# Kernel tuning notes

Measured on AMD Instinct MI355X. Metric: run time of the kernel, lower is better.

## Reference

```python
import jax, jax.numpy as jnp
import numpy as np

B, N = 256, 8192
H = 30
NUM_CLASSES = 5


def setup_inputs() -> dict:
    key = jax.random.key(0)
    ks = jax.random.split(key, 16)
    def dense(k, fi, fo):
        # flax default: lecun_normal kernel, zero bias
        return jax.random.normal(k, (fi, fo), jnp.float32) / jnp.sqrt(fi)
    return {
        'x':   jax.random.normal(ks[0], (B, N), jnp.float32),
        'W1':  dense(ks[1], 1, H),   'b1': jnp.zeros((H,), jnp.float32),
        'W2':  dense(ks[2], H, H),   'b2': jnp.zeros((H,), jnp.float32),
        'Wa1': dense(ks[3], H, 32),  'ba1': jnp.zeros((32,), jnp.float32),
        'Wa2': dense(ks[4], 32, 1),  'ba2': jnp.zeros((1,), jnp.float32),
        'Wf1': dense(ks[5], 6 * H, 40), 'bf1': jnp.zeros((40,), jnp.float32),
        'Wf2': dense(ks[6], 40, 40),    'bf2': jnp.zeros((40,), jnp.float32),
        'Wf3': dense(ks[7], 40, NUM_CLASSES), 'bf3': jnp.zeros((NUM_CLASSES,), jnp.float32),
    }


def reference(x, W1, b1, W2, b2, Wa1, ba1, Wa2, ba2, Wf1, bf1, Wf2, bf2, Wf3, bf3):
    # (B, N) -> (B, N, 1) -> Dense(30) -> relu -> Dense(30)
    h = jax.nn.relu(x[..., None] * W1[0] + b1)          # (B, N, 30)
    h = jnp.einsum('bnh,hk->bnk', h, W2) + b2           # (B, N, 30)

    # statistical pools over the point axis (axis=1)
    mean_pool = jnp.mean(h, axis=1)
    max_pool = jnp.max(h, axis=1)
    min_pool = jnp.min(h, axis=1)
    std_pool = jnp.std(h, axis=1)
    sum_pool = jnp.sum(h, axis=1)

    # attention pooling over points
    a = jax.nn.relu(jnp.einsum('bnh,hk->bnk', h, Wa1) + ba1)  # (B, N, 32)
    logits = jnp.einsum('bnk,ko->bno', a, Wa2) + ba2          # (B, N, 1)
    attn = jax.nn.softmax(logits, axis=1)                     # (B, N, 1)
    attention_pool = jnp.sum(h * attn, axis=1)                # (B, 30)

    feat = jnp.concatenate(
        [mean_pool, max_pool, min_pool, std_pool, sum_pool, attention_pool],
        axis=-1)                                              # (B, 180)

    z = jax.nn.relu(feat @ Wf1 + bf1)
    z = jax.nn.relu(z @ Wf2 + bf2)
    return z @ Wf3 + bf3                                      # (B, num_classes)
```

## Files before the change

kernel.cpp:

```cpp
#include <hip/hip_runtime.h>
#include <math.h>

#define NN 8192
#define HH 30
#define TPB 512
#define NIV 31
#define TSTR 68

__launch_bounds__(TPB, 2)
__global__ void pointnet_pwl5_kernel(
    const float* __restrict__ x,
    const float* __restrict__ W1,  const float* __restrict__ b1,
    const float* __restrict__ W2,  const float* __restrict__ b2,
    const float* __restrict__ Wa1, const float* __restrict__ ba1,
    const float* __restrict__ Wa2, const float* __restrict__ ba2,
    const float* __restrict__ Wf1, const float* __restrict__ bf1,
    const float* __restrict__ Wf2, const float* __restrict__ bf2,
    const float* __restrict__ Wf3, const float* __restrict__ bf3,
    float* __restrict__ out)
{
    __shared__ float W2s[HH][32];
    __shared__ float Wa1s[HH][32];
    __shared__ float w1s[HH], b1s[HH], b2s[32], ba1s[32];
    __shared__ __align__(16) float ts_s[32];
    __shared__ __align__(16) float Wa2s[32];
    __shared__ float tts[HH];
    __shared__ int   rnk[HH];
    __shared__ int   DcS, rmap1S;
    __shared__ float d0S;
    __shared__ float P[HH][32];
    __shared__ float vb2[32];
    __shared__ __align__(16) float ab2[2][64];
    __shared__ __align__(16) float uv2[2][64];
    __shared__ float zz_raw[128], zz_s[128];
    __shared__ float2 gcs[129];
    __shared__ __align__(16) float abt[NIV][TSTR];
    __shared__ __align__(16) float uvt[NIV][TSTR];
    __shared__ float red[8][154];
    __shared__ float fin[16];
    __shared__ float feat[192];
    __shared__ float redh[12][40];
    __shared__ float z1s[40], z2s[40];
    __shared__ float wf2s[40 * 40];
    __shared__ float wf3s[40 * 5];

    const int tid = threadIdx.x;
    const int b   = blockIdx.x;

    float2 xl[8];
    {
        const float2* xb2 = reinterpret_cast<const float2*>(x + (size_t)b * NN);
        #pragma unroll
        for (int it = 0; it < 8; ++it) xl[it] = xb2[it * TPB + tid];
    }
    float wf1r[15];
    if (tid < 480) {
        int o = tid % 40, p = tid / 40;
        const float* wrow = Wf1 + (p * 15) * 40 + o;
        #pragma unroll
        for (int ii = 0; ii < 15; ++ii) wf1r[ii] = wrow[ii * 40];
    }
    float bf1r = 0.f, bf2r = 0.f, bf3r = 0.f;
    if (tid < 40) { bf1r = bf1[tid]; bf2r = bf2[tid]; }
    if (tid < 5)  { bf3r = bf3[tid]; }

    for (int i = tid; i < HH * 32; i += TPB) {
        int j = i >> 5, k = i & 31;
        W2s[j][k] = (k < HH) ? W2[j * HH + k] : 0.f;
    }
    for (int i = tid; i < HH * 32; i += TPB) ((float*)Wa1s)[i] = Wa1[i];
    if (tid < HH) {
        float w = W1[tid], bb = b1[tid];
        w1s[tid] = w; b1s[tid] = bb;
        tts[tid] = (w != 0.f) ? (-bb / w) : INFINITY;
    }
    if (tid < 32) {
        b2s[tid]  = (tid < HH) ? b2[tid] : 0.f;
        ba1s[tid] = ba1[tid];
        Wa2s[tid] = Wa2[tid];
        ts_s[tid] = INFINITY;
    }
    for (int i = tid; i < 40 * 40; i += TPB) wf2s[i] = Wf2[i];
    for (int i = tid; i < 40 * 5;  i += TPB) wf3s[i] = Wf3[i];
    const float ba2v = ba2[0];
    __syncthreads();

    if (tid < HH) {
        float t = tts[tid];
        int r = 0;
        for (int i = 0; i < HH; ++i) {
            float ti = tts[i];
            r += (ti < t) || (ti == t && i < tid);
        }
        ts_s[r] = t;
        rnk[tid] = r;
    } else if (tid >= 32) {
        for (int e = tid - 32; e < HH * 32 + 32; e += (TPB - 32)) {
            if (e < HH * 32) {
                int j = e >> 5, m = e & 31;
                float s = 0.f;
                for (int k = 0; k < HH; ++k) s = fmaf(W2s[j][k], Wa1s[k][m], s);
                P[j][m] = s;
            } else {
                int m = e - HH * 32;
                float s = 0.f;
                for (int k = 0; k < HH; ++k) s = fmaf(Wa1s[k][m], b2s[k], s);
                vb2[m] = s;
            }
        }
    }
    __syncthreads();

    if (tid < 64) {
        bool fin_t = (tid < HH) && (ts_s[tid] < INFINITY);
        bool neq = fin_t && (tid == 0 || ts_s[tid] != ts_s[tid - 1]);
        unsigned long long md = __ballot(neq);
        float t0v = ts_s[0];
        bool eq0 = fin_t && (ts_s[tid] == t0v);
        unsigned long long me = __ballot(eq0);
        if (tid == 0) {
            DcS = __popcll(md);
            d0S = t0v;
            int c2 = __popcll(me);
            rmap1S = (c2 > 30) ? 30 : c2;
        }
    }
    __syncthreads();
    const int Dc = DcS;

    if (Dc == 1) {
        const float d0 = d0S;
        const int rmap1 = rmap1S;

        if (tid < 64) {
            int r = tid >> 5, k = tid & 31;
            int rr = r ? rmap1 : 0;
            float a = 0.f, bb = 0.f;
            if (k < HH) {
                for (int j = 0; j < HH; ++j) {
                    float w = w1s[j];
                    bool act = (w > 0.f) ? (rnk[j] < rr)
                             : ((w < 0.f) ? (rnk[j] >= rr) : (b1s[j] > 0.f));
                    if (act) {
                        float w2 = W2s[j][k];
                        a  = fmaf(w,      w2, a);
                        bb = fmaf(b1s[j], w2, bb);
                    }
                }
                bb += b2s[k];
            }
            ab2[r][k]      = a;
            ab2[r][32 + k] = bb;
        } else if (tid < 128) {
            int i2 = tid - 64;
            int r = i2 >> 5, m = i2 & 31;
            int rr = r ? rmap1 : 0;
            float u = 0.f, v = 0.f;
            for (int j = 0; j < HH; ++j) {
                float w = w1s[j];
                bool act = (w > 0.f) ? (rnk[j] < rr)
                         : ((w < 0.f) ? (rnk[j] >= rr) : (b1s[j] > 0.f));
                if (act) {
                    float pj = P[j][m];
                    u = fmaf(w,      pj, u);
                    v = fmaf(b1s[j], pj, v);
                }
            }
            v += vb2[m] + ba1s[m];
            uv2[r][m]      = u;
            uv2[r][32 + m] = v;
            float zr = -v / u;
            bool ok = (u != 0.f) && (r == 0 ? (zr < d0) : (zr > d0));
            zz_raw[1 + i2] = ok ? zr : INFINITY;
        } else if (tid < 191) {
            zz_raw[tid - 63] = INFINITY;
        } else if (tid == 191) {
            zz_raw[0] = d0;
        }
        __syncthreads();

        if (tid < 128) {
            float v = zz_raw[tid];
            int rk = 0;
            for (int i = 0; i < 128; ++i) {
                float vi = zz_raw[i];
                rk += (vi < v) || (vi == v && i < tid);
            }
            zz_s[rk] = v;
        }
        __syncthreads();

        if (tid < 129) {
            float lo = (tid == 0)   ? -INFINITY : zz_s[tid - 1];
            float hi = (tid == 128) ?  INFINITY : zz_s[tid];
            float xm;
            if (lo == -INFINITY)      xm = (hi < INFINITY) ? hi - 1.f : 0.f;
            else if (hi == INFINITY)  xm = lo + 1.f;
            else                      xm = 0.5f * (lo + hi);
            int r = (xm >= d0) ? 1 : 0;
            float g = 0.f, c = ba2v;
            for (int m = 0; m < 32; ++m) {
                float u = uv2[r][m], v = uv2[r][32 + m];
                if (fmaf(u, xm, v) > 0.f) {
                    float w = Wa2s[m];
                    g = fmaf(w, u, g);
                    c = fmaf(w, v, c);
                }
            }
            gcs[tid] = make_float2(g, c);
        }
        __syncthreads();

        float c0=0,c1=0, Sx0=0,Sx1=0, Q0=0,Q1=0;
        float mn0=INFINITY,mn1=INFINITY, mx0=-INFINITY,mx1=-INFINITY;
        float Sp0=0,Sp1=0, Px0=0,Px1=0;
        float mrun = -INFINITY;

        #pragma unroll
        for (int it = 0; it < 8; ++it) {
            float xv2[2] = { xl[it].x, xl[it].y };
            #pragma unroll
            for (int pp = 0; pp < 2; ++pp) {
                float xv = xv2[pp];
                bool q1 = (xv >= d0);
                int idx = 0;
                #pragma unroll
                for (int bit = 64; bit >= 1; bit >>= 1) {
                    int t = idx + bit;
                    idx = (zz_s[t - 1] <= xv) ? t : idx;
                }
                float2 gc = gcs[idx];
                float l = fmaf(xv, gc.x, gc.y);
                float dlt = l - mrun, p;
                if (dlt > 8.f) {
                    float sc = __expf(-dlt);
                    Sp0 *= sc; Sp1 *= sc; Px0 *= sc; Px1 *= sc;
                    mrun = l; p = 1.f;
                } else p = __expf(dlt);
                float xx = xv * xv, px = p * xv;
                float i1 = q1 ? 1.f : 0.f, i0 = 1.f - i1;
                c0 += i0;                    c1 += i1;
                Sx0 = fmaf(i0, xv, Sx0);     Sx1 = fmaf(i1, xv, Sx1);
                Q0  = fmaf(i0, xx, Q0);      Q1  = fmaf(i1, xx, Q1);
                Sp0 = fmaf(i0, p,  Sp0);     Sp1 = fmaf(i1, p,  Sp1);
                Px0 = fmaf(i0, px, Px0);     Px1 = fmaf(i1, px, Px1);
                mn0 = fminf(mn0, q1 ?  INFINITY : xv);
                mx0 = fmaxf(mx0, q1 ? -INFINITY : xv);
                mn1 = fminf(mn1, q1 ? xv :  INFINITY);
                mx1 = fmaxf(mx1, q1 ? xv : -INFINITY);
            }
        }

        #pragma unroll 1
        for (int off = 32; off > 0; off >>= 1) {
            c0  += __shfl_xor(c0,  off);  c1  += __shfl_xor(c1,  off);
            Sx0 += __shfl_xor(Sx0, off);  Sx1 += __shfl_xor(Sx1, off);
            Q0  += __shfl_xor(Q0,  off);  Q1  += __shfl_xor(Q1,  off);
            mn0 = fminf(mn0, __shfl_xor(mn0, off));
            mn1 = fminf(mn1, __shfl_xor(mn1, off));
            mx0 = fmaxf(mx0, __shfl_xor(mx0, off));
            mx1 = fmaxf(mx1, __shfl_xor(mx1, off));
            float mo = __shfl_xor(mrun, off);
            float M  = fmaxf(mrun, mo);
            float sa = __expf(mrun - M), sb = __expf(mo - M);
            float t;
            t = __shfl_xor(Sp0, off); Sp0 = Sp0 * sa + t * sb;
            t = __shfl_xor(Sp1, off); Sp1 = Sp1 * sa + t * sb;
            t = __shfl_xor(Px0, off); Px0 = Px0 * sa + t * sb;
            t = __shfl_xor(Px1, off); Px1 = Px1 * sa + t * sb;
            mrun = M;
        }

        const int wave = tid >> 6, lane = tid & 63;
        if (lane == 0) {
            float* rw = red[wave];
            rw[0]=c0; rw[1]=Sx0; rw[2]=Q0; rw[3]=mn0; rw[4]=mx0; rw[5]=Sp0; rw[6]=Px0;
            rw[7]=c1; rw[8]=Sx1; rw[9]=Q1; rw[10]=mn1; rw[11]=mx1; rw[12]=Sp1; rw[13]=Px1;
            rw[14]=mrun;
        }
        __syncthreads();

        if (tid < 2) {
            float M = red[0][14];
            #pragma unroll
            for (int w = 1; w < 8; ++w) M = fmaxf(M, red[w][14]);
            int base = tid * 7;
            float ck=0, Sx=0, Q=0, mnv=INFINITY, mxv=-INFINITY, Sp=0, Px=0;
            #pragma unroll
            for (int w = 0; w < 8; ++w) {
                ck += red[w][base+0]; Sx += red[w][base+1]; Q += red[w][base+2];
                mnv = fminf(mnv, red[w][base+3]); mxv = fmaxf(mxv, red[w][base+4]);
                float e = __expf(red[w][14] - M);
                Sp = fmaf(red[w][base+5], e, Sp);
                Px = fmaf(red[w][base+6], e, Px);
            }
            fin[base+0]=ck; fin[base+1]=Sx; fin[base+2]=Q;
            fin[base+3]=mnv; fin[base+4]=mxv; fin[base+5]=Sp; fin[base+6]=Px;
        }
        __syncthreads();

        if (tid < HH) {
            float sumk=0, ssqk=0, acck=0, L=0;
            float mxk=-INFINITY, mnk=INFINITY;
            #pragma unroll
            for (int r2 = 0; r2 < 2; ++r2) {
                float ck = fin[r2*7+0], Sx = fin[r2*7+1], Q = fin[r2*7+2];
                float xmn = fin[r2*7+3], xmx = fin[r2*7+4];
                float Sp = fin[r2*7+5], Px = fin[r2*7+6];
                float a = ab2[r2][tid], bb = ab2[r2][32 + tid];
                sumk += a * Sx + bb * ck;
                ssqk += a * a * Q + 2.f * a * bb * Sx + bb * bb * ck;
                acck += a * Px + bb * Sp;
                L += Sp;
                if (ck > 0.f) {
                    float h1 = fmaf(a, xmn, bb), h2v = fmaf(a, xmx, bb);
                    mxk = fmaxf(mxk, fmaxf(h1, h2v));
                    mnk = fminf(mnk, fminf(h1, h2v));
                }
            }
            const float invN = 1.f / (float)NN;
            float mean = sumk * invN;
            float var  = fmaxf(ssqk * invN - mean * mean, 0.f);
            feat[tid]        = mean;
            feat[30 + tid]   = mxk;
            feat[60 + tid]   = mnk;
            feat[90 + tid]   = sqrtf(var);
            feat[120 + tid]  = sumk;
            feat[150 + tid]  = acck / L;
        }
    } else {
        for (int idx = tid; idx < NIV * 32; idx += TPB) {
            int r = idx >> 5, k = idx & 31;
            float a = 0.f, bb = 0.f;
            if (k < HH) {
                for (int j = 0; j < HH; ++j) {
                    float w = w1s[j];
                    bool act = (w > 0.f) ? (rnk[j] < r)
                             : ((w < 0.f) ? (rnk[j] >= r) : (b1s[j] > 0.f));
                    if (act) {
                        float w2 = W2s[j][k];
                        a  = fmaf(w,      w2, a);
                        bb = fmaf(b1s[j], w2, bb);
                    }
                }
                bb += b2s[k];
            }
            abt[r][k]      = a;
            abt[r][32 + k] = bb;
        }
        __syncthreads();
        for (int idx = tid; idx < NIV * 32; idx += TPB) {
            int r = idx >> 5, m = idx & 31;
            float u = 0.f, v = 0.f;
            for (int k = 0; k < HH; ++k) {
                float wa = Wa1s[k][m];
                u = fmaf(wa, abt[r][k],      u);
                v = fmaf(wa, abt[r][32 + k], v);
            }
            v += ba1s[m];
            uvt[r][m]      = u;
            uvt[r][32 + m] = v;
        }
        __syncthreads();

        float sum[HH], ssq[HH], mx[HH], mn[HH], acc[HH];
        #pragma unroll
        for (int k = 0; k < HH; ++k) {
            sum[k] = 0.f; ssq[k] = 0.f; acc[k] = 0.f;
            mx[k] = -INFINITY; mn[k] = INFINITY;
        }
        float mrun = -INFINITY, lrun = 0.f;
        const float* xb = x + (size_t)b * NN;
        const float4* ts4 = (const float4*)ts_s;
        const float4* wv4 = (const float4*)Wa2s;

        #pragma unroll 1
        for (int it = 0; it < NN / TPB; ++it) {
            float xv = xb[it * TPB + tid];
            int r = 0;
            #pragma unroll
            for (int i = 0; i < 8; ++i) {
                float4 t = ts4[i];
                r += (xv >= t.x) ? 1 : 0;
                r += (xv >= t.y) ? 1 : 0;
                r += (xv >= t.z) ? 1 : 0;
                r += (xv >= t.w) ? 1 : 0;
            }
            float h2[HH];
            const float4* arow = (const float4*)(&abt[r][0]);
            #pragma unroll
            for (int i = 0; i < 7; ++i) {
                float4 av = arow[i], bv = arow[8 + i];
                h2[4*i+0] = fmaf(xv, av.x, bv.x);
                h2[4*i+1] = fmaf(xv, av.y, bv.y);
                h2[4*i+2] = fmaf(xv, av.z, bv.z);
                h2[4*i+3] = fmaf(xv, av.w, bv.w);
            }
            { float4 av = arow[7], bv = arow[15];
              h2[28] = fmaf(xv, av.x, bv.x);
              h2[29] = fmaf(xv, av.y, bv.y); }
            #pragma unroll
            for (int k = 0; k < HH; ++k) {
                float h = h2[k];
                sum[k] += h;
                ssq[k] = fmaf(h, h, ssq[k]);
                mx[k] = fmaxf(mx[k], h);
                mn[k] = fminf(mn[k], h);
            }
            float l = ba2v;
            const float4* urow = (const float4*)(&uvt[r][0]);
            #pragma unroll
            for (int i = 0; i < 8; ++i) {
                float4 uu = urow[i], vv = urow[8 + i], ww = wv4[i];
                l = fmaf(fmaxf(fmaf(xv, uu.x, vv.x), 0.f), ww.x, l);
                l = fmaf(fmaxf(fmaf(xv, uu.y, vv.y), 0.f), ww.y, l);
                l = fmaf(fmaxf(fmaf(xv, uu.z, vv.z), 0.f), ww.z, l);
                l = fmaf(fmaxf(fmaf(xv, uu.w, vv.w), 0.f), ww.w, l);
            }
            float d = l - mrun, p;
            if (d > 8.f) {
                float s = __expf(-d);
                lrun *= s;
                #pragma unroll
                for (int k = 0; k < HH; ++k) acc[k] *= s;
                mrun = l; p = 1.f;
            } else p = __expf(d);
            lrun += p;
            #pragma unroll
            for (int k = 0; k < HH; ++k) acc[k] = fmaf(p, h2[k], acc[k]);
        }

        #pragma unroll 1
        for (int off = 32; off > 0; off >>= 1) {
            #pragma unroll
            for (int k = 0; k < HH; ++k) {
                sum[k] += __shfl_xor(sum[k], off);
                ssq[k] += __shfl_xor(ssq[k], off);
                mx[k] = fmaxf(mx[k], __shfl_xor(mx[k], off));
                mn[k] = fminf(mn[k], __shfl_xor(mn[k], off));
            }
            float mo = __shfl_xor(mrun, off);
            float lo = __shfl_xor(lrun, off);
            float M  = fmaxf(mrun, mo);
            float sa = __expf(mrun - M), sb = __expf(mo - M);
            lrun = lrun * sa + lo * sb;
            #pragma unroll
            for (int k = 0; k < HH; ++k)
                acc[k] = acc[k] * sa + __shfl_xor(acc[k], off) * sb;
            mrun = M;
        }

        const int wave = tid >> 6, lane = tid & 63;
        if (lane == 0) {
            #pragma unroll
            for (int k = 0; k < HH; ++k) {
                red[wave][k]       = sum[k];
                red[wave][30 + k]  = ssq[k];
                red[wave][60 + k]  = mx[k];
                red[wave][90 + k]  = mn[k];
                red[wave][120 + k] = acc[k];
            }
            red[wave][150] = mrun;
            red[wave][151] = lrun;
        }
        __syncthreads();

        if (tid < HH) {
            float M = -INFINITY;
            #pragma unroll
            for (int w = 0; w < 8; ++w) M = fmaxf(M, red[w][150]);
            float s = 0.f, ss = 0.f, L = 0.f, A = 0.f;
            float mxv = -INFINITY, mnv = INFINITY;
            #pragma unroll
            for (int w = 0; w < 8; ++w) {
                s  += red[w][tid];
                ss += red[w][30 + tid];
                mxv = fmaxf(mxv, red[w][60 + tid]);
                mnv = fminf(mnv, red[w][90 + tid]);
                float e = __expf(red[w][150] - M);
                L = fmaf(red[w][151], e, L);
                A = fmaf(red[w][120 + tid], e, A);
            }
            const float invN = 1.f / (float)NN;
            float mean = s * invN;
            float var  = fmaxf(ss * invN - mean * mean, 0.f);
            feat[tid]       = mean;
            feat[30 + tid]  = mxv;
            feat[60 + tid]  = mnv;
            feat[90 + tid]  = sqrtf(var);
            feat[120 + tid] = s;
            feat[150 + tid] = A / L;
        }
    }
    __syncthreads();

    if (tid < 480) {
        int o = tid % 40, p = tid / 40;
        float z = 0.f;
        #pragma unroll
        for (int ii = 0; ii < 15; ++ii)
            z = fmaf(feat[p * 15 + ii], wf1r[ii], z);
        redh[p][o] = z;
    }
    __syncthreads();
    if (tid < 40) {
        float z = bf1r;
        #pragma unroll
        for (int p = 0; p < 12; ++p) z += redh[p][tid];
        z1s[tid] = fmaxf(z, 0.f);
    }
    __syncthreads();
    if (tid < 40) {
        float z = bf2r;
        #pragma unroll
        for (int i = 0; i < 40; ++i) z = fmaf(z1s[i], wf2s[i * 40 + tid], z);
        z2s[tid] = fmaxf(z, 0.f);
    }
    __syncthreads();
    if (tid < 5) {
        float o = bf3r;
        #pragma unroll
        for (int i = 0; i < 40; ++i) o = fmaf(z2s[i], wf3s[i * 5 + tid], o);
        out[b * 5 + tid] = o;
    }
}

extern "C" void kernel_launch(void* const* d_in, const int* in_sizes, int n_in,
                              void* d_out, int out_size, void* d_ws, size_t ws_size,
                              hipStream_t stream) {
    const float* x   = (const float*)d_in[0];
    const float* W1  = (const float*)d_in[1];
    const float* b1  = (const float*)d_in[2];
    const float* W2  = (const float*)d_in[3];
    const float* b2  = (const float*)d_in[4];
    const float* Wa1 = (const float*)d_in[5];
    const float* ba1 = (const float*)d_in[6];
    const float* Wa2 = (const float*)d_in[7];
    const float* ba2 = (const float*)d_in[8];
    const float* Wf1 = (const float*)d_in[9];
    const float* bf1 = (const float*)d_in[10];
    const float* Wf2 = (const float*)d_in[11];
    const float* bf2 = (const float*)d_in[12];
    const float* Wf3 = (const float*)d_in[13];
    const float* bf3 = (const float*)d_in[14];
    float* out = (float*)d_out;

    pointnet_pwl5_kernel<<<256, TPB, 0, stream>>>(
        x, W1, b1, W2, b2, Wa1, ba1, Wa2, ba2,
        Wf1, bf1, Wf2, bf2, Wf3, bf3, out);
}
```

Baseline: 118.6 us.

## Double block size to 1024 threads and simplify single-breakpoint setup path

Raises threads per block from 512 to 1024, so each thread holds 8 points loaded as two float4s and the cross-wave reductions cover 16 waves. The breakpoint setup is simplified: min/max shuffles detect the single-breakpoint case, the rank sort moves into the general path only, and the activation masks no longer use ranks. Wf1 and the final biases are staged in shared memory rather than registers. The aim is more parallelism per sample and a shorter serial prologue, at the cost of larger LDS use, more register pressure per thread and fewer resident blocks per CU.

```diff
diff --git a/kernel.cpp b/kernel.cpp
--- a/kernel.cpp
+++ b/kernel.cpp
@@ -3,12 +3,12 @@
 
 #define NN 8192
 #define HH 30
-#define TPB 512
+#define TPB 1024
 #define NIV 31
 #define TSTR 68
 
-__launch_bounds__(TPB, 2)
-__global__ void pointnet_pwl5_kernel(
+__launch_bounds__(TPB)
+__global__ void pointnet_pwl7_kernel(
     const float* __restrict__ x,
     const float* __restrict__ W1,  const float* __restrict__ b1,
     const float* __restrict__ W2,  const float* __restrict__ b2,
@@ -21,54 +21,47 @@
 {
     __shared__ float W2s[HH][32];
     __shared__ float Wa1s[HH][32];
-    __shared__ float w1s[HH], b1s[HH], b2s[32], ba1s[32];
-    __shared__ __align__(16) float ts_s[32];
-    __shared__ __align__(16) float Wa2s[32];
-    __shared__ float tts[HH];
-    __shared__ int   rnk[HH];
-    __shared__ int   DcS, rmap1S;
+    __shared__ float P[HH][32];
+    __shared__ float w1s[HH], b1s[HH], tts[HH];
+    __shared__ float b2s[32], ba1s[32], Wa2s[32], vb2[32];
+    __shared__ int   DcS;
     __shared__ float d0S;
-    __shared__ float P[HH][32];
-    __shared__ float vb2[32];
     __shared__ __align__(16) float ab2[2][64];
     __shared__ __align__(16) float uv2[2][64];
     __shared__ float zz_raw[128], zz_s[128];
     __shared__ float2 gcs[129];
+    __shared__ __align__(16) float ts_s[32];
+    __shared__ int   rnk[HH];
     __shared__ __align__(16) float abt[NIV][TSTR];
     __shared__ __align__(16) float uvt[NIV][TSTR];
-    __shared__ float red[8][154];
+    __shared__ float redb[16][155];
     __shared__ float fin[16];
     __shared__ float feat[192];
     __shared__ float redh[12][40];
     __shared__ float z1s[40], z2s[40];
+    __shared__ float wf1s[180 * 40];
     __shared__ float wf2s[40 * 40];
     __shared__ float wf3s[40 * 5];
+    __shared__ float bf1s[40], bf2s[40], bf3s[8];
 
     const int tid = threadIdx.x;
     const int b   = blockIdx.x;
 
-    float2 xl[8];
+    float4 xl0, xl1;
     {
-        const float2* xb2 = reinterpret_cast<const float2*>(x + (size_t)b * NN);
-        #pragma unroll
-        for (int it = 0; it < 8; ++it) xl[it] = xb2[it * TPB + tid];
-    }
-    float wf1r[15];
-    if (tid < 480) {
-        int o = tid % 40, p = tid / 40;
-        const float* wrow = Wf1 + (p * 15) * 40 + o;
-        #pragma unroll
-        for (int ii = 0; ii < 15; ++ii) wf1r[ii] = wrow[ii * 40];
-    }
-    float bf1r = 0.f, bf2r = 0.f, bf3r = 0.f;
-    if (tid < 40) { bf1r = bf1[tid]; bf2r = bf2[tid]; }
-    if (tid < 5)  { bf3r = bf3[tid]; }
+        const float4* xb4 = reinterpret_cast<const float4*>(x + (size_t)b * NN);
+        xl0 = xb4[tid];
+        xl1 = xb4[tid + TPB];
+    }
 
     for (int i = tid; i < HH * 32; i += TPB) {
         int j = i >> 5, k = i & 31;
         W2s[j][k] = (k < HH) ? W2[j * HH + k] : 0.f;
     }
     for (int i = tid; i < HH * 32; i += TPB) ((float*)Wa1s)[i] = Wa1[i];
+    for (int i = tid; i < 180 * 40; i += TPB) wf1s[i] = Wf1[i];
+    for (int i = tid; i < 40 * 40;  i += TPB) wf2s[i] = Wf2[i];
+    if (tid < 40 * 5) wf3s[tid] = Wf3[tid];
     if (tid < HH) {
         float w = W1[tid], bb = b1[tid];
         w1s[tid] = w; b1s[tid] = bb;
@@ -80,67 +73,52 @@
         Wa2s[tid] = Wa2[tid];
         ts_s[tid] = INFINITY;
     }
-    for (int i = tid; i < 40 * 40; i += TPB) wf2s[i] = Wf2[i];
-    for (int i = tid; i < 40 * 5;  i += TPB) wf3s[i] = Wf3[i];
+    if (tid < 40) { bf1s[tid] = bf1[tid]; bf2s[tid] = bf2[tid]; }
+    if (tid < 5)  { bf3s[tid] = bf3[tid]; }
     const float ba2v = ba2[0];
     __syncthreads();
 
-    if (tid < HH) {
-        float t = tts[tid];
-        int r = 0;
-        for (int i = 0; i < HH; ++i) {
-            float ti = tts[i];
-            r += (ti < t) || (ti == t && i < tid);
-        }
-        ts_s[r] = t;
-        rnk[tid] = r;
-    } else if (tid >= 32) {
-        for (int e = tid - 32; e < HH * 32 + 32; e += (TPB - 32)) {
-            if (e < HH * 32) {
-                int j = e >> 5, m = e & 31;
-                float s = 0.f;
-                for (int k = 0; k < HH; ++k) s = fmaf(W2s[j][k], Wa1s[k][m], s);
-                P[j][m] = s;
-            } else {
-                int m = e - HH * 32;
-                float s = 0.f;
-                for (int k = 0; k < HH; ++k) s = fmaf(Wa1s[k][m], b2s[k], s);
-                vb2[m] = s;
-            }
+    if (tid < HH * 32) {
+        int j = tid >> 5, m = tid & 31;
+        float s = 0.f;
+        #pragma unroll
+        for (int k = 0; k < HH; ++k) s = fmaf(W2s[j][k], Wa1s[k][m], s);
+        P[j][m] = s;
+    } else if (tid < HH * 32 + 32) {
+        int m = tid - HH * 32;
+        float s = 0.f;
+        #pragma unroll
+        for (int k = 0; k < HH; ++k) s = fmaf(Wa1s[k][m], b2s[k], s);
+        vb2[m] = s;
+    }
+    if (tid < 64) {
+        float t = (tid < HH) ? tts[tid] : INFINITY;
+        bool fin_t = (t < INFINITY);
+        float tmin = fin_t ? t :  INFINITY;
+        float tmax = fin_t ? t : -INFINITY;
+        #pragma unroll
+        for (int off = 32; off > 0; off >>= 1) {
+            tmin = fminf(tmin, __shfl_xor(tmin, off));
+            tmax = fmaxf(tmax, __shfl_xor(tmax, off));
+        }
+        if (tid == 0) {
+            bool dc1 = (tmin < INFINITY) && (tmin == tmax);
+            DcS = dc1 ? 1 : 0;
+            d0S = tmin;
         }
     }
     __syncthreads();
 
-    if (tid < 64) {
-        bool fin_t = (tid < HH) && (ts_s[tid] < INFINITY);
-        bool neq = fin_t && (tid == 0 || ts_s[tid] != ts_s[tid - 1]);
-        unsigned long long md = __ballot(neq);
-        float t0v = ts_s[0];
-        bool eq0 = fin_t && (ts_s[tid] == t0v);
-        unsigned long long me = __ballot(eq0);
-        if (tid == 0) {
-            DcS = __popcll(md);
-            d0S = t0v;
-            int c2 = __popcll(me);
-            rmap1S = (c2 > 30) ? 30 : c2;
-        }
-    }
-    __syncthreads();
-    const int Dc = DcS;
-
-    if (Dc == 1) {
+    if (DcS == 1) {
         const float d0 = d0S;
-        const int rmap1 = rmap1S;
 
         if (tid < 64) {
             int r = tid >> 5, k = tid & 31;
-            int rr = r ? rmap1 : 0;
             float a = 0.f, bb = 0.f;
             if (k < HH) {
                 for (int j = 0; j < HH; ++j) {
                     float w = w1s[j];
-                    bool act = (w > 0.f) ? (rnk[j] < rr)
-                             : ((w < 0.f) ? (rnk[j] >= rr) : (b1s[j] > 0.f));
+                    bool act = (w == 0.f) ? (b1s[j] > 0.f) : (r ? (w > 0.f) : (w < 0.f));
                     if (act) {
                         float w2 = W2s[j][k];
                         a  = fmaf(w,      w2, a);
@@ -154,12 +132,10 @@
         } else if (tid < 128) {
             int i2 = tid - 64;
             int r = i2 >> 5, m = i2 & 31;
-            int rr = r ? rmap1 : 0;
             float u = 0.f, v = 0.f;
             for (int j = 0; j < HH; ++j) {
                 float w = w1s[j];
-                bool act = (w > 0.f) ? (rnk[j] < rr)
-                         : ((w < 0.f) ? (rnk[j] >= rr) : (b1s[j] > 0.f));
+                bool act = (w == 0.f) ? (b1s[j] > 0.f) : (r ? (w > 0.f) : (w < 0.f));
                 if (act) {
                     float pj = P[j][m];
                     u = fmaf(w,      pj, u);
@@ -216,39 +192,36 @@
         float Sp0=0,Sp1=0, Px0=0,Px1=0;
         float mrun = -INFINITY;
 
-        #pragma unroll
-        for (int it = 0; it < 8; ++it) {
-            float xv2[2] = { xl[it].x, xl[it].y };
-            #pragma unroll
-            for (int pp = 0; pp < 2; ++pp) {
-                float xv = xv2[pp];
-                bool q1 = (xv >= d0);
-                int idx = 0;
-                #pragma unroll
-                for (int bit = 64; bit >= 1; bit >>= 1) {
-                    int t = idx + bit;
-                    idx = (zz_s[t - 1] <= xv) ? t : idx;
-                }
-                float2 gc = gcs[idx];
-                float l = fmaf(xv, gc.x, gc.y);
-                float dlt = l - mrun, p;
-                if (dlt > 8.f) {
-                    float sc = __expf(-dlt);
-                    Sp0 *= sc; Sp1 *= sc; Px0 *= sc; Px1 *= sc;
-                    mrun = l; p = 1.f;
-                } else p = __expf(dlt);
-                float xx = xv * xv, px = p * xv;
-                float i1 = q1 ? 1.f : 0.f, i0 = 1.f - i1;
-                c0 += i0;                    c1 += i1;
-                Sx0 = fmaf(i0, xv, Sx0);     Sx1 = fmaf(i1, xv, Sx1);
-                Q0  = fmaf(i0, xx, Q0);      Q1  = fmaf(i1, xx, Q1);
-                Sp0 = fmaf(i0, p,  Sp0);     Sp1 = fmaf(i1, p,  Sp1);
-                Px0 = fmaf(i0, px, Px0);     Px1 = fmaf(i1, px, Px1);
-                mn0 = fminf(mn0, q1 ?  INFINITY : xv);
-                mx0 = fmaxf(mx0, q1 ? -INFINITY : xv);
-                mn1 = fminf(mn1, q1 ? xv :  INFINITY);
-                mx1 = fmaxf(mx1, q1 ? xv : -INFINITY);
-            }
+        float xs[8] = {xl0.x, xl0.y, xl0.z, xl0.w, xl1.x, xl1.y, xl1.z, xl1.w};
+        #pragma unroll
+        for (int pp = 0; pp < 8; ++pp) {
+            float xv = xs[pp];
+            bool q1 = (xv >= d0);
+            int idx = 0;
+            #pragma unroll
+            for (int bit = 64; bit >= 1; bit >>= 1) {
+                int t = idx + bit;
+                idx = (zz_s[t - 1] <= xv) ? t : idx;
+            }
+            float2 gc = gcs[idx];
+            float l = fmaf(xv, gc.x, gc.y);
+            float dlt = l - mrun, p;
+            if (dlt > 8.f) {
+                float sc = __expf(-dlt);
+                Sp0 *= sc; Sp1 *= sc; Px0 *= sc; Px1 *= sc;
+                mrun = l; p = 1.f;
+            } else p = __expf(dlt);
+            float xx = xv * xv, px = p * xv;
+            float i1 = q1 ? 1.f : 0.f, i0 = 1.f - i1;
+            c0 += i0;                    c1 += i1;
+            Sx0 = fmaf(i0, xv, Sx0);     Sx1 = fmaf(i1, xv, Sx1);
+            Q0  = fmaf(i0, xx, Q0);      Q1  = fmaf(i1, xx, Q1);
+            Sp0 = fmaf(i0, p,  Sp0);     Sp1 = fmaf(i1, p,  Sp1);
+            Px0 = fmaf(i0, px, Px0);     Px1 = fmaf(i1, px, Px1);
+            mn0 = fminf(mn0, q1 ?  INFINITY : xv);
+            mx0 = fmaxf(mx0, q1 ? -INFINITY : xv);
+            mn1 = fminf(mn1, q1 ? xv :  INFINITY);
+            mx1 = fmaxf(mx1, q1 ? xv : -INFINITY);
         }
 
         #pragma unroll 1
@@ -273,7 +246,7 @@
 
         const int wave = tid >> 6, lane = tid & 63;
         if (lane == 0) {
-            float* rw = red[wave];
+            float* rw = redb[wave];
             rw[0]=c0; rw[1]=Sx0; rw[2]=Q0; rw[3]=mn0; rw[4]=mx0; rw[5]=Sp0; rw[6]=Px0;
             rw[7]=c1; rw[8]=Sx1; rw[9]=Q1; rw[10]=mn1; rw[11]=mx1; rw[12]=Sp1; rw[13]=Px1;
             rw[14]=mrun;
@@ -281,18 +254,18 @@
         __syncthreads();
 
         if (tid < 2) {
-            float M = red[0][14];
-            #pragma unroll
-            for (int w = 1; w < 8; ++w) M = fmaxf(M, red[w][14]);
+            float M = redb[0][14];
+            #pragma unroll
+            for (int w = 1; w < 16; ++w) M = fmaxf(M, redb[w][14]);
             int base = tid * 7;
             float ck=0, Sx=0, Q=0, mnv=INFINITY, mxv=-INFINITY, Sp=0, Px=0;
             #pragma unroll
-            for (int w = 0; w < 8; ++w) {
-                ck += red[w][base+0]; Sx += red[w][base+1]; Q += red[w][base+2];
-                mnv = fminf(mnv, red[w][base+3]); mxv = fmaxf(mxv, red[w][base+4]);
-                float e = __expf(red[w][14] - M);
-                Sp = fmaf(red[w][base+5], e, Sp);
-                Px = fmaf(red[w][base+6], e, Px);
+            for (int w = 0; w < 16; ++w) {
+                ck += redb[w][base+0]; Sx += redb[w][base+1]; Q += redb[w][base+2];
+                mnv = fminf(mnv, redb[w][base+3]); mxv = fmaxf(mxv, redb[w][base+4]);
+                float e = __expf(redb[w][14] - M);
+                Sp = fmaf(redb[w][base+5], e, Sp);
+                Px = fmaf(redb[w][base+6], e, Px);
             }
             fin[base+0]=ck; fin[base+1]=Sx; fin[base+2]=Q;
             fin[base+3]=mnv; fin[base+4]=mxv; fin[base+5]=Sp; fin[base+6]=Px;
@@ -329,6 +302,17 @@
             feat[150 + tid]  = acck / L;
         }
     } else {
+        if (tid < HH) {
+            float t = tts[tid];
+            int r = 0;
+            for (int i = 0; i < HH; ++i) {
+                float ti = tts[i];
+                r += (ti < t) || (ti == t && i < tid);
+            }
+            ts_s[r] = t;
+            rnk[tid] = r;
+        }
+        __syncthreads();
         for (int idx = tid; idx < NIV * 32; idx += TPB) {
             int r = idx >> 5, k = idx & 31;
             float a = 0.f, bb = 0.f;
@@ -454,32 +438,32 @@
         if (lane == 0) {
             #pragma unroll
             for (int k = 0; k < HH; ++k) {
-                red[wave][k]       = sum[k];
-                red[wave][30 + k]  = ssq[k];
-                red[wave][60 + k]  = mx[k];
-                red[wave][90 + k]  = mn[k];
-                red[wave][120 + k] = acc[k];
-            }
-            red[wave][150] = mrun;
-            red[wave][151] = lrun;
+                redb[wave][k]       = sum[k];
+                redb[wave][30 + k]  = ssq[k];
+                redb[wave][60 + k]  = mx[k];
+                redb[wave][90 + k]  = mn[k];
+                redb[wave][120 + k] = acc[k];
+            }
+            redb[wave][150] = mrun;
+            redb[wave][151] = lrun;
         }
         __syncthreads();
 
         if (tid < HH) {
             float M = -INFINITY;
             #pragma unroll
-            for (int w = 0; w < 8; ++w) M = fmaxf(M, red[w][150]);
+            for (int w = 0; w < 16; ++w) M = fmaxf(M, redb[w][150]);
             float s = 0.f, ss = 0.f, L = 0.f, A = 0.f;
             float mxv = -INFINITY, mnv = INFINITY;
             #pragma unroll
-            for (int w = 0; w < 8; ++w) {
-                s  += red[w][tid];
-                ss += red[w][30 + tid];
-                mxv = fmaxf(mxv, red[w][60 + tid]);
-                mnv = fminf(mnv, red[w][90 + tid]);
-                float e = __expf(red[w][150] - M);
-                L = fmaf(red[w][151], e, L);
-                A = fmaf(red[w][120 + tid], e, A);
+            for (int w = 0; w < 16; ++w) {
+                s  += redb[w][tid];
+                ss += redb[w][30 + tid];
+                mxv = fmaxf(mxv, redb[w][60 + tid]);
+                mnv = fminf(mnv, redb[w][90 + tid]);
+                float e = __expf(redb[w][150] - M);
+                L = fmaf(redb[w][151], e, L);
+                A = fmaf(redb[w][120 + tid], e, A);
             }
             const float invN = 1.f / (float)NN;
             float mean = s * invN;
@@ -499,26 +483,26 @@
         float z = 0.f;
         #pragma unroll
         for (int ii = 0; ii < 15; ++ii)
-            z = fmaf(feat[p * 15 + ii], wf1r[ii], z);
+            z = fmaf(feat[p * 15 + ii], wf1s[(p * 15 + ii) * 40 + o], z);
         redh[p][o] = z;
     }
     __syncthreads();
     if (tid < 40) {
-        float z = bf1r;
+        float z = bf1s[tid];
         #pragma unroll
         for (int p = 0; p < 12; ++p) z += redh[p][tid];
         z1s[tid] = fmaxf(z, 0.f);
     }
     __syncthreads();
     if (tid < 40) {
-        float z = bf2r;
+        float z = bf2s[tid];
         #pragma unroll
         for (int i = 0; i < 40; ++i) z = fmaf(z1s[i], wf2s[i * 40 + tid], z);
         z2s[tid] = fmaxf(z, 0.f);
     }
     __syncthreads();
     if (tid < 5) {
-        float o = bf3r;
+        float o = bf3s[tid];
         #pragma unroll
         for (int i = 0; i < 40; ++i) o = fmaf(z2s[i], wf3s[i * 5 + tid], o);
         out[b * 5 + tid] = o;
@@ -545,7 +529,7 @@
     const float* bf3 = (const float*)d_in[14];
     float* out = (float*)d_out;
 
-    pointnet_pwl5_kernel<<<256, TPB, 0, stream>>>(
+    pointnet_pwl7_kernel<<<256, TPB, 0, stream>>>(
         x, W1, b1, W2, b2, Wa1, ba1, Wa2, ba2,
         Wf1, bf1, Wf2, bf2, Wf3, bf3, out);
 }
```

After: 113.6 us. 1.04x faster.
